# Kernel tuning notes

Hardware: AMD Instinct MI355X
Metric: run time of the kernel (lower is better)

The kernel has to match this reference:

```python
import jax, jax.numpy as jnp
import numpy as np

J = 4
K = 16  # kernel_size
M_ORDER = 4
PAD = K // 2


def _make_filters():
    t = np.linspace(-2.0, 2.0, K)
    z = 1.0 - 1j * t
    psi = (1.0 / z) ** (M_ORDER + 1)
    psi = psi - psi.mean()
    phi = np.exp(-2.0 * t ** 2)
    phi = phi / phi.sum()
    psi = psi / np.linalg.norm(psi) / np.sqrt(2.0)
    phi = phi / np.linalg.norm(phi) / np.sqrt(2.0)
    return (psi.real.astype(np.float32), psi.imag.astype(np.float32),
            phi.astype(np.float32))


def setup_inputs() -> dict:
    key = jax.random.key(0)
    k1, k2 = jax.random.split(key)
    B, T = 32, 524288
    x_real = jax.random.normal(k1, (B, T), dtype=jnp.float32)
    x_imag = jax.random.normal(k2, (B, T), dtype=jnp.float32)
    pr, pi, ph = _make_filters()
    return {
        'x_real': x_real, 'x_imag': x_imag,
        'psi_real': jnp.asarray(pr), 'psi_imag': jnp.asarray(pi),
        'phi': jnp.asarray(ph),
    }


def _conv_same(x, w, L):
    # x: (B, L) real; w: (K,) real. torch F.conv1d = cross-correlation, 'same'-ish
    # padding K//2 gives length L+1, trimmed back to L (as in the torch code).
    y = jax.lax.conv_general_dilated(x[:, None, :], w[None, None, :],
                                     window_strides=(1,),
                                     padding=[(PAD, PAD)])
    return y[:, 0, :L]


def reference(x_real, x_imag, psi_real, psi_imag, phi):
    x = x_real + 1j * x_imag  # complex64
    coefficients = []
    for j in range(J):
        L = x.shape[-1]
        xr, xi = x.real, x.imag
        # low-pass (complex signal * real filter), then decimate by 2
        s = _conv_same(xr, phi, L) + 1j * _conv_same(xi, phi, L)
        coefficients.append(s[..., ::2])
        # complex band-pass conv: (a+bi)*(c+di)
        rr = _conv_same(xr, psi_real, L)
        ri = _conv_same(xr, psi_imag, L)
        ir = _conv_same(xi, psi_real, L)
        ii = _conv_same(xi, psi_imag, L)
        u = (rr - ii) + 1j * (ri + ir)
        # modulus rectifier (cast back to complex, imag = 0)
        w = jnp.abs(u).astype(u.dtype)
        x = w[..., ::2]
        if x.shape[-1] < K:
            break
    return tuple(coefficients)
```

## Files before the change

kernel.cpp:

```cpp
#include <hip/hip_runtime.h>


using f16x2 = __attribute__((ext_vector_type(2))) __fp16;

static __device__ __forceinline__ uint packh2(float a, float b) {
    f16x2 r = __builtin_amdgcn_cvt_pkrtz(a, b);
    return __builtin_bit_cast(uint, r);
}
static __device__ __forceinline__ uint pkadd(uint a, uint b) {
    f16x2 x = __builtin_bit_cast(f16x2, a);
    f16x2 y = __builtin_bit_cast(f16x2, b);
    f16x2 r = x + y;
    return __builtin_bit_cast(uint, r);
}
static __device__ __forceinline__ float dot2(f16x2 f, uint w, float c) {
#if __has_builtin(__builtin_amdgcn_fdot2)
    return __builtin_amdgcn_fdot2(f, __builtin_bit_cast(f16x2, w), c, false);
#else
    f16x2 h = __builtin_bit_cast(f16x2, w);
    return fmaf((float)f.x, (float)h.x, fmaf((float)f.y, (float)h.y, c));
#endif
}

constexpr int S1   = 2048;
constexpr int H1   = 56;
constexpr int NT1  = S1 + 2 * H1;
constexpr int NPIN = 2168;
constexpr int NTH  = 256;

__global__ __launch_bounds__(NTH, 6) void hst_fused_kernel(
    const float* __restrict__ xr, const float* __restrict__ xi,
    const float* __restrict__ psi_r, const float* __restrict__ psi_i,
    const float* __restrict__ phi,
    float* __restrict__ out,
    long o0, long o1, long o2, long o3,
    int L0, int h0, int h1, int h2, int h3)
{
    __shared__ __align__(16) uint REP[NPIN];
    __shared__ __align__(16) uint IMP[NPIN];
    __shared__ __align__(16) uint X1P[1080];
    __shared__ __align__(16) uint X2P[536];
    __shared__ __align__(16) uint X3P[264];

    const int tid  = threadIdx.x;
    const int wv   = tid >> 6;
    const int lane = tid & 63;
    const int gx   = blockIdx.x;
    const int b    = blockIdx.y;
    const int s    = gx * S1;
    const bool edge = (gx == 0) || (gx == (int)gridDim.x - 1);
    const int X0   = 2 * (s - H1) - 8;

    const float* rowr = xr + (size_t)b * (size_t)L0;
    const float* rowi = xi + (size_t)b * (size_t)L0;

    f16x2 FH[8], FR[8], FI[8], FS[8];
    #pragma unroll
    for (int j = 0; j < 8; ++j) {
        FH[j] = __builtin_amdgcn_cvt_pkrtz(phi[2*j],   phi[2*j+1]);
        FR[j] = __builtin_amdgcn_cvt_pkrtz(psi_r[2*j], psi_r[2*j+1]);
        FI[j] = __builtin_amdgcn_cvt_pkrtz(psi_i[2*j], psi_i[2*j+1]);
        FS[j] = __builtin_amdgcn_cvt_pkrtz(psi_r[2*j] + psi_i[2*j],
                                           psi_r[2*j+1] + psi_i[2*j+1]);
    }

    if (!edge) {
        const float4* pr4 = reinterpret_cast<const float4*>(rowr + X0);
        const float4* pi4 = reinterpret_cast<const float4*>(rowi + X0);
        #pragma unroll
        for (int n = 0; n < 4; ++n) {
            const int i = tid + n * NTH;
            float4 a = pr4[i];
            float4 c = pi4[i];
            uint2 wa; wa.x = packh2(a.x, a.y); wa.y = packh2(a.z, a.w);
            uint2 wc; wc.x = packh2(c.x, c.y); wc.y = packh2(c.z, c.w);
            *reinterpret_cast<uint2*>(&REP[2*i]) = wa;
            *reinterpret_cast<uint2*>(&IMP[2*i]) = wc;
        }
        if (lane < 15) {
            const int i = 1024 + 15 * wv + lane;
            float4 a = pr4[i];
            float4 c = pi4[i];
            uint2 wa; wa.x = packh2(a.x, a.y); wa.y = packh2(a.z, a.w);
            uint2 wc; wc.x = packh2(c.x, c.y); wc.y = packh2(c.z, c.w);
            *reinterpret_cast<uint2*>(&REP[2*i]) = wa;
            *reinterpret_cast<uint2*>(&IMP[2*i]) = wc;
        }
    } else {
        for (int i = tid; i < NPIN; i += NTH) {
            int g0 = X0 + 2 * i;
            float r0 = (g0   >= 0 && g0   < L0) ? rowr[g0]   : 0.0f;
            float r1 = (g0+1 >= 0 && g0+1 < L0) ? rowr[g0+1] : 0.0f;
            float i0 = (g0   >= 0 && g0   < L0) ? rowi[g0]   : 0.0f;
            float i1 = (g0+1 >= 0 && g0+1 < L0) ? rowi[g0+1] : 0.0f;
            REP[i] = packh2(r0, r1);
            IMP[i] = packh2(i0, i1);
        }
    }
    __syncthreads();

    #pragma unroll
    for (int n = 0; n < 2; ++n) {
        const int g = tid + n * NTH;
        const uint4* wp = reinterpret_cast<const uint4*>(&REP[4*g]);
        uint4 a0 = wp[0], a1 = wp[1], a2 = wp[2];
        const uint4* ip = reinterpret_cast<const uint4*>(&IMP[4*g]);
        uint4 c0v = ip[0], c1v = ip[1], c2v = ip[2];
        const uint wr[12] = {a0.x,a0.y,a0.z,a0.w, a1.x,a1.y,a1.z,a1.w, a2.x,a2.y,a2.z,a2.w};
        const uint wi[12] = {c0v.x,c0v.y,c0v.z,c0v.w, c1v.x,c1v.y,c1v.z,c1v.w, c2v.x,c2v.y,c2v.z,c2v.w};
        uint ws[12];
        #pragma unroll
        for (int j = 0; j < 12; ++j) ws[j] = pkadd(wr[j], wi[j]);

        float phv[4], mag[4];
        #pragma unroll
        for (int r = 0; r < 4; ++r) {
            float sh = 0.f, A = 0.f, Bv = 0.f, C = 0.f;
            #pragma unroll
            for (int j = 0; j < 8; ++j) {
                sh = dot2(FH[j], wr[r+j], sh);
                A  = dot2(FR[j], wr[r+j], A);
                Bv = dot2(FI[j], wi[r+j], Bv);
                C  = dot2(FS[j], ws[r+j], C);
            }
            float ur = A - Bv;
            float ui = C - (A + Bv);
            float m2 = sqrtf(fmaf(ur, ur, ui * ui));
            if (edge) {
                int m = s - H1 + 4*g + r;
                m2 = (m >= 0 && m < h0) ? m2 : 0.0f;
            }
            mag[r] = m2;
            phv[r] = sh;
        }
        uint2 xp; xp.x = packh2(mag[0], mag[1]); xp.y = packh2(mag[2], mag[3]);
        *reinterpret_cast<uint2*>(&X1P[2*g]) = xp;

        if (g >= 14) {
            long m0 = (long)s - H1 + 4*g;
            float4 st; st.x = phv[0]; st.y = phv[1]; st.z = phv[2]; st.w = phv[3];
            *reinterpret_cast<float4*>(out + o0 + (long)b * h0 + m0) = st;
        }
    }

    if (lane < 28) {
        const int h  = 28 * wv + lane;
        const int lm = S1 + h;
        uint wr8[8], wi8[8], ws8[8];
        #pragma unroll
        for (int j = 0; j < 8; ++j) {
            wr8[j] = REP[lm + j]; wi8[j] = IMP[lm + j];
            ws8[j] = pkadd(wr8[j], wi8[j]);
        }
        float sh = 0.f, A = 0.f, Bv = 0.f, C = 0.f;
        #pragma unroll
        for (int j = 0; j < 8; ++j) {
            sh = dot2(FH[j], wr8[j], sh);
            A  = dot2(FR[j], wr8[j], A);
            Bv = dot2(FI[j], wi8[j], Bv);
            C  = dot2(FS[j], ws8[j], C);
        }
        float ur = A - Bv;
        float ui = C - (A + Bv);
        float m2 = sqrtf(fmaf(ur, ur, ui * ui));
        if (edge) {
            int m = s - H1 + lm;
            m2 = (m >= 0 && m < h0) ? m2 : 0.0f;
        }
        reinterpret_cast<__fp16*>(X1P)[lm] = (__fp16)m2;
        if (h < 56)
            out[o0 + (long)b * h0 + (s + S1 - H1 + h)] = sh;
    }
    __syncthreads();

    {
        const int t = tid;
        const uint4* wp = reinterpret_cast<const uint4*>(&X1P[4*t]);
        uint4 a0 = wp[0], a1 = wp[1];
        uint2 u2 = *reinterpret_cast<const uint2*>(&X1P[4*t+8]);
        uint  w10 = X1P[4*t+10];
        const uint w[11] = {a0.x,a0.y,a0.z,a0.w, a1.x,a1.y,a1.z,a1.w, u2.x,u2.y, w10};

        float phv[4], mag[4];
        #pragma unroll
        for (int r = 0; r < 4; ++r) {
            float sh = 0.f, ur = 0.f, ui = 0.f;
            #pragma unroll
            for (int j = 0; j < 8; ++j) {
                sh = dot2(FH[j], w[r+j], sh);
                ur = dot2(FR[j], w[r+j], ur);
                ui = dot2(FI[j], w[r+j], ui);
            }
            float m2 = sqrtf(fmaf(ur, ur, ui * ui));
            const int q = s/2 - 24 + 4*t + r;
            if (edge) m2 = (q >= 0 && q < h1) ? m2 : 0.0f;
            mag[r] = m2;
            phv[r] = sh;
        }
        uint2 xp; xp.x = packh2(mag[0], mag[1]); xp.y = packh2(mag[2], mag[3]);
        *reinterpret_cast<uint2*>(&X2P[2*t]) = xp;

        if (t >= 6) {
            long q0 = (long)s/2 - 24 + 4*t;
            float4 st; st.x = phv[0]; st.y = phv[1]; st.z = phv[2]; st.w = phv[3];
            *reinterpret_cast<float4*>(out + o1 + (long)b * h1 + q0) = st;
        }
    }
    if (lane < 12) {
        const int h   = 12 * wv + lane;
        const int pos = 1024 + h;
        uint w8[8];
        #pragma unroll
        for (int j = 0; j < 8; ++j) w8[j] = X1P[pos + j];
        float sh = 0.f, ur = 0.f, ui = 0.f;
        #pragma unroll
        for (int j = 0; j < 8; ++j) {
            sh = dot2(FH[j], w8[j], sh);
            ur = dot2(FR[j], w8[j], ur);
            ui = dot2(FI[j], w8[j], ui);
        }
        float m2 = sqrtf(fmaf(ur, ur, ui * ui));
        const int q = s/2 - 24 + pos;
        if (edge) m2 = (q >= 0 && q < h1) ? m2 : 0.0f;
        reinterpret_cast<__fp16*>(X2P)[pos] = (__fp16)m2;
        if (h < 24)
            out[o1 + (long)b * h1 + q] = sh;
    }
    __syncthreads();

    {
        const int t = tid;
        uint2 u0 = *reinterpret_cast<const uint2*>(&X2P[2*t]);
        uint2 u1 = *reinterpret_cast<const uint2*>(&X2P[2*t+2]);
        uint2 u2 = *reinterpret_cast<const uint2*>(&X2P[2*t+4]);
        uint2 u3 = *reinterpret_cast<const uint2*>(&X2P[2*t+6]);
        uint  w8 = X2P[2*t+8];
        const uint w[9] = {u0.x,u0.y,u1.x,u1.y,u2.x,u2.y,u3.x,u3.y,w8};

        float phv[2], mag[2];
        #pragma unroll
        for (int r = 0; r < 2; ++r) {
            float sh = 0.f, ur = 0.f, ui = 0.f;
            #pragma unroll
            for (int j = 0; j < 8; ++j) {
                sh = dot2(FH[j], w[r+j], sh);
                ur = dot2(FR[j], w[r+j], ur);
                ui = dot2(FI[j], w[r+j], ui);
            }
            float m2 = sqrtf(fmaf(ur, ur, ui * ui));
            const int p = s/4 - 8 + 2*t + r;
            if (edge) m2 = (p >= 0 && p < h2) ? m2 : 0.0f;
            mag[r] = m2;
            phv[r] = sh;
        }
        X3P[t] = packh2(mag[0], mag[1]);
        if (t >= 4) {
            long p0 = (long)s/4 - 8 + 2*t;
            *reinterpret_cast<float2*>(out + o2 + (long)b * h2 + p0) =
                make_float2(phv[0], phv[1]);
        }
    }
    if (lane < 4) {
        const int h   = 4 * wv + lane;
        const int pos = 512 + h;
        uint w8[8];
        #pragma unroll
        for (int j = 0; j < 8; ++j) w8[j] = X2P[pos + j];
        float sh = 0.f, ur = 0.f, ui = 0.f;
        #pragma unroll
        for (int j = 0; j < 8; ++j) {
            sh = dot2(FH[j], w8[j], sh);
            ur = dot2(FR[j], w8[j], ur);
            ui = dot2(FI[j], w8[j], ui);
        }
        float m2 = sqrtf(fmaf(ur, ur, ui * ui));
        const int p = s/4 - 8 + pos;
        if (edge) m2 = (p >= 0 && p < h2) ? m2 : 0.0f;
        reinterpret_cast<__fp16*>(X3P)[pos] = (__fp16)m2;
        if (h < 8)
            out[o2 + (long)b * h2 + p] = sh;
    }
    __syncthreads();

    {
        float sh = 0.f;
        #pragma unroll
        for (int j = 0; j < 8; ++j)
            sh = dot2(FH[j], X3P[tid + j], sh);
        out[o3 + (long)b * h3 + (s/8 + tid)] = sh;
    }
}

extern "C" void kernel_launch(void* const* d_in, const int* in_sizes, int n_in,
                              void* d_out, int out_size, void* d_ws, size_t ws_size,
                              hipStream_t stream) {
    const float* xr    = (const float*)d_in[0];
    const float* xi    = (const float*)d_in[1];
    const float* psi_r = (const float*)d_in[2];
    const float* psi_i = (const float*)d_in[3];
    const float* phi   = (const float*)d_in[4];
    float* out = (float*)d_out;

    const int B  = 32;
    const int T  = in_sizes[0] / B;
    const int L0 = T;
    const int h0 = L0 / 2;
    const int h1 = h0 / 2;
    const int h2 = h1 / 2;
    const int h3 = h2 / 2;

    const long o0 = 0;
    const long o1 = o0 + (long)B * h0;
    const long o2 = o1 + (long)B * h1;
    const long o3 = o2 + (long)B * h2;

    dim3 blk(NTH, 1, 1);
    dim3 grd(h0 / S1, B, 1);
    hipLaunchKernelGGL(hst_fused_kernel, grd, blk, 0, stream,
                       xr, xi, psi_r, psi_i, phi,
                       out, o0, o1, o2, o3,
                       L0, h0, h1, h2, h3);
}
```

Measured before the change: 46.04 us.

## Split fused scattering kernel into level-0 and level-1..3 kernels via workspace

```diff
diff --git a/kernel.cpp b/kernel.cpp
--- a/kernel.cpp
+++ b/kernel.cpp
@@ -24,9 +24,286 @@
 
 constexpr int S1   = 2048;
 constexpr int H1   = 56;
-constexpr int NT1  = S1 + 2 * H1;
+constexpr int NTH  = 256;
+
+constexpr int NPIN1 = 2056;
+constexpr int NLD1  = NPIN1 / 2;
+
+__global__ __launch_bounds__(NTH, 6) void hst_l0_kernel(
+    const float* __restrict__ xr, const float* __restrict__ xi,
+    const float* __restrict__ psi_r, const float* __restrict__ psi_i,
+    const float* __restrict__ phi,
+    float* __restrict__ out, uint* __restrict__ x1w,
+    int L0, int h0)
+{
+    __shared__ __align__(16) uint REP[NPIN1];
+    __shared__ __align__(16) uint IMP[NPIN1];
+
+    const int tid  = threadIdx.x;
+    const int wv   = tid >> 6;
+    const int lane = tid & 63;
+    const int gx   = blockIdx.x;
+    const int b    = blockIdx.y;
+    const int s    = gx * S1;
+    const bool edge = (gx == 0) || (gx == (int)gridDim.x - 1);
+    const int X0   = 2 * s - 8;
+
+    const float* rowr = xr + (size_t)b * (size_t)L0;
+    const float* rowi = xi + (size_t)b * (size_t)L0;
+
+    f16x2 FH[8], FR[8], FI[8], FS[8];
+    #pragma unroll
+    for (int j = 0; j < 8; ++j) {
+        FH[j] = __builtin_amdgcn_cvt_pkrtz(phi[2*j],   phi[2*j+1]);
+        FR[j] = __builtin_amdgcn_cvt_pkrtz(psi_r[2*j], psi_r[2*j+1]);
+        FI[j] = __builtin_amdgcn_cvt_pkrtz(psi_i[2*j], psi_i[2*j+1]);
+        FS[j] = __builtin_amdgcn_cvt_pkrtz(psi_r[2*j] + psi_i[2*j],
+                                           psi_r[2*j+1] + psi_i[2*j+1]);
+    }
+
+    if (!edge) {
+        const float4* pr4 = reinterpret_cast<const float4*>(rowr + X0);
+        const float4* pi4 = reinterpret_cast<const float4*>(rowi + X0);
+        #pragma unroll
+        for (int n = 0; n < 4; ++n) {
+            const int i = tid + n * NTH;
+            float4 a = pr4[i];
+            float4 c = pi4[i];
+            uint2 wa; wa.x = packh2(a.x, a.y); wa.y = packh2(a.z, a.w);
+            uint2 wc; wc.x = packh2(c.x, c.y); wc.y = packh2(c.z, c.w);
+            *reinterpret_cast<uint2*>(&REP[2*i]) = wa;
+            *reinterpret_cast<uint2*>(&IMP[2*i]) = wc;
+        }
+        if (lane < 1) {
+            const int i = 1024 + wv;
+            float4 a = pr4[i];
+            float4 c = pi4[i];
+            uint2 wa; wa.x = packh2(a.x, a.y); wa.y = packh2(a.z, a.w);
+            uint2 wc; wc.x = packh2(c.x, c.y); wc.y = packh2(c.z, c.w);
+            *reinterpret_cast<uint2*>(&REP[2*i]) = wa;
+            *reinterpret_cast<uint2*>(&IMP[2*i]) = wc;
+        }
+    } else {
+        for (int i = tid; i < NPIN1; i += NTH) {
+            int g0 = X0 + 2 * i;
+            float r0 = (g0   >= 0 && g0   < L0) ? rowr[g0]   : 0.0f;
+            float r1 = (g0+1 >= 0 && g0+1 < L0) ? rowr[g0+1] : 0.0f;
+            float i0 = (g0   >= 0 && g0   < L0) ? rowi[g0]   : 0.0f;
+            float i1 = (g0+1 >= 0 && g0+1 < L0) ? rowi[g0+1] : 0.0f;
+            REP[i] = packh2(r0, r1);
+            IMP[i] = packh2(i0, i1);
+        }
+    }
+    __syncthreads();
+
+    #pragma unroll
+    for (int n = 0; n < 2; ++n) {
+        const int g = tid + n * NTH;
+        const uint4* wp = reinterpret_cast<const uint4*>(&REP[4*g]);
+        uint4 a0 = wp[0], a1 = wp[1], a2 = wp[2];
+        const uint4* ip = reinterpret_cast<const uint4*>(&IMP[4*g]);
+        uint4 c0v = ip[0], c1v = ip[1], c2v = ip[2];
+        const uint wr[12] = {a0.x,a0.y,a0.z,a0.w, a1.x,a1.y,a1.z,a1.w, a2.x,a2.y,a2.z,a2.w};
+        const uint wi[12] = {c0v.x,c0v.y,c0v.z,c0v.w, c1v.x,c1v.y,c1v.z,c1v.w, c2v.x,c2v.y,c2v.z,c2v.w};
+        uint ws12[12];
+        #pragma unroll
+        for (int j = 0; j < 12; ++j) ws12[j] = pkadd(wr[j], wi[j]);
+
+        float phv[4], mag[4];
+        #pragma unroll
+        for (int r = 0; r < 4; ++r) {
+            float sh = 0.f, A = 0.f, Bv = 0.f, C = 0.f;
+            #pragma unroll
+            for (int j = 0; j < 8; ++j) {
+                sh = dot2(FH[j], wr[r+j], sh);
+                A  = dot2(FR[j], wr[r+j], A);
+                Bv = dot2(FI[j], wi[r+j], Bv);
+                C  = dot2(FS[j], ws12[r+j], C);
+            }
+            float ur = A - Bv;
+            float ui = C - (A + Bv);
+            mag[r] = sqrtf(fmaf(ur, ur, ui * ui));
+            phv[r] = sh;
+        }
+        long m0 = (long)s + 4*g;
+        float4 st; st.x = phv[0]; st.y = phv[1]; st.z = phv[2]; st.w = phv[3];
+        *reinterpret_cast<float4*>(out + (long)b * h0 + m0) = st;
+        uint2 xp; xp.x = packh2(mag[0], mag[1]); xp.y = packh2(mag[2], mag[3]);
+        *reinterpret_cast<uint2*>(&x1w[(size_t)b * (h0/2) + s/2 + 2*g]) = xp;
+    }
+}
+
+__global__ __launch_bounds__(NTH, 6) void hst_l123_kernel(
+    const uint* __restrict__ x1w,
+    const float* __restrict__ psi_r, const float* __restrict__ psi_i,
+    const float* __restrict__ phi,
+    float* __restrict__ out,
+    long o1, long o2, long o3,
+    int h0, int h1, int h2, int h3)
+{
+    __shared__ __align__(16) uint X1P[1080];
+    __shared__ __align__(16) uint X2P[536];
+    __shared__ __align__(16) uint X3P[264];
+
+    const int tid  = threadIdx.x;
+    const int wv   = tid >> 6;
+    const int lane = tid & 63;
+    const int gx   = blockIdx.x;
+    const int b    = blockIdx.y;
+    const int s    = gx * S1;
+    const bool edge = (gx == 0) || (gx == (int)gridDim.x - 1);
+    const int W0   = s/2 - 28;
+
+    const uint* row = x1w + (size_t)b * (h0/2);
+
+    f16x2 FH[8], FR[8], FI[8];
+    #pragma unroll
+    for (int j = 0; j < 8; ++j) {
+        FH[j] = __builtin_amdgcn_cvt_pkrtz(phi[2*j],   phi[2*j+1]);
+        FR[j] = __builtin_amdgcn_cvt_pkrtz(psi_r[2*j], psi_r[2*j+1]);
+        FI[j] = __builtin_amdgcn_cvt_pkrtz(psi_i[2*j], psi_i[2*j+1]);
+    }
+
+    if (!edge) {
+        const uint4* src = reinterpret_cast<const uint4*>(row + W0);
+        {
+            uint4 v = src[tid];
+            *reinterpret_cast<uint4*>(&X1P[4*tid]) = v;
+        }
+        if (lane < 4) {
+            const int i = 256 + 4*wv + lane;
+            if (i < 270) {
+                uint4 v = src[i];
+                *reinterpret_cast<uint4*>(&X1P[4*i]) = v;
+            }
+        }
+    } else {
+        for (int i = tid; i < 1080; i += NTH) {
+            int W = W0 + i;
+            X1P[i] = (W >= 0 && W < h0/2) ? row[W] : 0u;
+        }
+    }
+    __syncthreads();
+
+    {
+        const int t = tid;
+        const uint4* wp = reinterpret_cast<const uint4*>(&X1P[4*t]);
+        uint4 a0 = wp[0], a1 = wp[1];
+        uint2 u2 = *reinterpret_cast<const uint2*>(&X1P[4*t+8]);
+        uint  w10 = X1P[4*t+10];
+        const uint w[11] = {a0.x,a0.y,a0.z,a0.w, a1.x,a1.y,a1.z,a1.w, u2.x,u2.y, w10};
+
+        float phv[4], mag[4];
+        #pragma unroll
+        for (int r = 0; r < 4; ++r) {
+            float sh = 0.f, ur = 0.f, ui = 0.f;
+            #pragma unroll
+            for (int j = 0; j < 8; ++j) {
+                sh = dot2(FH[j], w[r+j], sh);
+                ur = dot2(FR[j], w[r+j], ur);
+                ui = dot2(FI[j], w[r+j], ui);
+            }
+            float m2 = sqrtf(fmaf(ur, ur, ui * ui));
+            const int q = s/2 - 24 + 4*t + r;
+            if (edge) m2 = (q >= 0 && q < h1) ? m2 : 0.0f;
+            mag[r] = m2;
+            phv[r] = sh;
+        }
+        uint2 xp; xp.x = packh2(mag[0], mag[1]); xp.y = packh2(mag[2], mag[3]);
+        *reinterpret_cast<uint2*>(&X2P[2*t]) = xp;
+
+        if (t >= 6) {
+            long q0 = (long)s/2 - 24 + 4*t;
+            float4 st; st.x = phv[0]; st.y = phv[1]; st.z = phv[2]; st.w = phv[3];
+            *reinterpret_cast<float4*>(out + o1 + (long)b * h1 + q0) = st;
+        }
+    }
+    if (lane < 12) {
+        const int h   = 12 * wv + lane;
+        const int pos = 1024 + h;
+        uint w8[8];
+        #pragma unroll
+        for (int j = 0; j < 8; ++j) w8[j] = X1P[pos + j];
+        float sh = 0.f, ur = 0.f, ui = 0.f;
+        #pragma unroll
+        for (int j = 0; j < 8; ++j) {
+            sh = dot2(FH[j], w8[j], sh);
+            ur = dot2(FR[j], w8[j], ur);
+            ui = dot2(FI[j], w8[j], ui);
+        }
+        float m2 = sqrtf(fmaf(ur, ur, ui * ui));
+        const int q = s/2 - 24 + pos;
+        if (edge) m2 = (q >= 0 && q < h1) ? m2 : 0.0f;
+        reinterpret_cast<__fp16*>(X2P)[pos] = (__fp16)m2;
+        if (h < 24)
+            out[o1 + (long)b * h1 + q] = sh;
+    }
+    __syncthreads();
+
+    {
+        const int t = tid;
+        uint2 u0 = *reinterpret_cast<const uint2*>(&X2P[2*t]);
+        uint2 u1 = *reinterpret_cast<const uint2*>(&X2P[2*t+2]);
+        uint2 u2 = *reinterpret_cast<const uint2*>(&X2P[2*t+4]);
+        uint2 u3 = *reinterpret_cast<const uint2*>(&X2P[2*t+6]);
+        uint  w8 = X2P[2*t+8];
+        const uint w[9] = {u0.x,u0.y,u1.x,u1.y,u2.x,u2.y,u3.x,u3.y,w8};
+
+        float phv[2], mag[2];
+        #pragma unroll
+        for (int r = 0; r < 2; ++r) {
+            float sh = 0.f, ur = 0.f, ui = 0.f;
+            #pragma unroll
+            for (int j = 0; j < 8; ++j) {
+                sh = dot2(FH[j], w[r+j], sh);
+                ur = dot2(FR[j], w[r+j], ur);
+                ui = dot2(FI[j], w[r+j], ui);
+            }
+            float m2 = sqrtf(fmaf(ur, ur, ui * ui));
+            const int p = s/4 - 8 + 2*t + r;
+            if (edge) m2 = (p >= 0 && p < h2) ? m2 : 0.0f;
+            mag[r] = m2;
+            phv[r] = sh;
+        }
+        X3P[t] = packh2(mag[0], mag[1]);
+        if (t >= 4) {
+            long p0 = (long)s/4 - 8 + 2*t;
+            *reinterpret_cast<float2*>(out + o2 + (long)b * h2 + p0) =
+                make_float2(phv[0], phv[1]);
+        }
+    }
+    if (lane < 4) {
+        const int h   = 4 * wv + lane;
+        const int pos = 512 + h;
+        uint w8[8];
+        #pragma unroll
+        for (int j = 0; j < 8; ++j) w8[j] = X2P[pos + j];
+        float sh = 0.f, ur = 0.f, ui = 0.f;
+        #pragma unroll
+        for (int j = 0; j < 8; ++j) {
+            sh = dot2(FH[j], w8[j], sh);
+            ur = dot2(FR[j], w8[j], ur);
+            ui = dot2(FI[j], w8[j], ui);
+        }
+        float m2 = sqrtf(fmaf(ur, ur, ui * ui));
+        const int p = s/4 - 8 + pos;
+        if (edge) m2 = (p >= 0 && p < h2) ? m2 : 0.0f;
+        reinterpret_cast<__fp16*>(X3P)[pos] = (__fp16)m2;
+        if (h < 8)
+            out[o2 + (long)b * h2 + p] = sh;
+    }
+    __syncthreads();
+
+    {
+        float sh = 0.f;
+        #pragma unroll
+        for (int j = 0; j < 8; ++j)
+            sh = dot2(FH[j], X3P[tid + j], sh);
+        out[o3 + (long)b * h3 + (s/8 + tid)] = sh;
+    }
+}
+
 constexpr int NPIN = 2168;
-constexpr int NTH  = 256;
 
 __global__ __launch_bounds__(NTH, 6) void hst_fused_kernel(
     const float* __restrict__ xr, const float* __restrict__ xi,
@@ -108,9 +385,9 @@
         uint4 c0v = ip[0], c1v = ip[1], c2v = ip[2];
         const uint wr[12] = {a0.x,a0.y,a0.z,a0.w, a1.x,a1.y,a1.z,a1.w, a2.x,a2.y,a2.z,a2.w};
         const uint wi[12] = {c0v.x,c0v.y,c0v.z,c0v.w, c1v.x,c1v.y,c1v.z,c1v.w, c2v.x,c2v.y,c2v.z,c2v.w};
-        uint ws[12];
-        #pragma unroll
-        for (int j = 0; j < 12; ++j) ws[j] = pkadd(wr[j], wi[j]);
+        uint ws12[12];
+        #pragma unroll
+        for (int j = 0; j < 12; ++j) ws12[j] = pkadd(wr[j], wi[j]);
 
         float phv[4], mag[4];
         #pragma unroll
@@ -121,7 +398,7 @@
                 sh = dot2(FH[j], wr[r+j], sh);
                 A  = dot2(FR[j], wr[r+j], A);
                 Bv = dot2(FI[j], wi[r+j], Bv);
-                C  = dot2(FS[j], ws[r+j], C);
+                C  = dot2(FS[j], ws12[r+j], C);
             }
             float ur = A - Bv;
             float ui = C - (A + Bv);
@@ -314,10 +591,22 @@
     const long o2 = o1 + (long)B * h1;
     const long o3 = o2 + (long)B * h2;
 
+    const size_t x1_bytes = (size_t)B * (size_t)(h0 / 2) * 4u;
+
     dim3 blk(NTH, 1, 1);
     dim3 grd(h0 / S1, B, 1);
-    hipLaunchKernelGGL(hst_fused_kernel, grd, blk, 0, stream,
-                       xr, xi, psi_r, psi_i, phi,
-                       out, o0, o1, o2, o3,
-                       L0, h0, h1, h2, h3);
+
+    if (ws_size >= x1_bytes) {
+        uint* x1w = (uint*)d_ws;
+        hipLaunchKernelGGL(hst_l0_kernel, grd, blk, 0, stream,
+                           xr, xi, psi_r, psi_i, phi, out, x1w, L0, h0);
+        hipLaunchKernelGGL(hst_l123_kernel, grd, blk, 0, stream,
+                           x1w, psi_r, psi_i, phi, out, o1, o2, o3,
+                           h0, h1, h2, h3);
+    } else {
+        hipLaunchKernelGGL(hst_fused_kernel, grd, blk, 0, stream,
+                           xr, xi, psi_r, psi_i, phi,
+                           out, o0, o1, o2, o3,
+                           L0, h0, h1, h2, h3);
+    }
 }
```

Result: slower. 53.70 us (+16.6%).
